# Performance work log

Hardware: AMD Instinct MI355X
Metric: run time of the kernel (lower is better)

The kernel has to match this reference:

```python
import jax, jax.numpy as jnp
import numpy as np

CUBE_LEN = 512
EQU_H = 1024
EQU_W = 2 * EQU_H
EQU_COUNT = 4
CHANNELS = 3


def _rodrigues(r):
    th = np.linalg.norm(r)
    if th < 1e-12:
        return np.eye(3)
    k = r / th
    K = np.array([[0.0, -k[2], k[1]], [k[2], 0.0, -k[0]], [-k[1], k[0], 0.0]])
    return np.eye(3) + np.sin(th) * K + (1.0 - np.cos(th)) * (K @ K)


def _build_lut(L, equ_h):
    # Identical math to Cube2Equirec.__init__/_intersection, fused into
    # per-pixel face id + per-pixel cube-face pixel coordinates (u, v).
    equ_w = equ_h * 2
    theta = (np.arange(equ_w) / (equ_w - 1) - 0.5) * 2 * np.pi
    phi = (np.arange(equ_h) / (equ_h - 1) - 0.5) * np.pi
    theta, phi = np.meshgrid(theta, phi)
    x = np.sin(theta) * np.cos(phi)
    y = np.sin(phi)
    z = np.cos(theta) * np.cos(phi)
    xyz = np.stack([x, y, z], axis=-1)  # [H, W, 3]
    planes = np.array([[0, 0, 1, -1], [1, 0, 0, -1], [0, 0, 1, 1],
                       [1, 0, 0, 1], [0, 1, 0, 1], [0, 1, 0, -1]], dtype=np.float64)
    r_lst = np.array([[0, 0, 0], [0, -0.5, 0], [0, 1, 0],
                      [0, 0.5, 0], [-0.5, 0, 0], [0.5, 0, 0]]) * np.pi
    f = L / 2.0
    K = np.array([[f, 0, (L - 1) / 2.0], [0, f, (L - 1) / 2.0], [0, 0, 1]])
    R_lst = np.stack([_rodrigues(r) for r in r_lst])  # [6, 3, 3]

    abc = planes[:, :3]
    with np.errstate(divide='ignore'):
        depth = -planes[:, 3][None, None, :] / (xyz @ abc.T)  # [H, W, 6]
    depth[depth < 0] = np.inf
    arg = np.argmin(depth, axis=-1)            # per-pixel face id
    dmin = np.min(depth, axis=-1)
    pts = dmin[..., None] * xyz                # intersection points
    Rs = R_lst[arg]                            # [H, W, 3, 3]
    proj = np.einsum('ij,hwjk,hwk->hwi', K, Rs, pts)  # K @ R @ pts
    uv = np.clip(proj[..., :2] / proj[..., 2:3], 0, L - 1)
    return uv.astype(np.float32), arg.astype(np.int32)


def setup_inputs() -> dict:
    key = jax.random.key(0)
    x = jax.random.normal(key, (6 * EQU_COUNT, CHANNELS, CUBE_LEN, CUBE_LEN),
                          dtype=jnp.float32)
    uv_np, face_np = _build_lut(CUBE_LEN, EQU_H)
    return {"x": x, "uv": jnp.asarray(uv_np), "face_idx": jnp.asarray(face_np)}


def _cube2equirec(x, uv, face_idx):
    # x: [6*E, C, L, L]; grid_sample(mode='bilinear', align_corners=True)
    # with grid = (uv/(L-1) - 0.5)*2 samples exactly at pixel coords uv.
    E6, C, L, _ = x.shape
    E = E6 // 6
    xr = x.reshape(E, 6, C, L, L)
    H, W = face_idx.shape
    f = face_idx.reshape(-1)                 # [N]
    u = uv[..., 0].reshape(-1)               # [N], in [0, L-1]
    v = uv[..., 1].reshape(-1)

    x0 = jnp.clip(jnp.floor(u).astype(jnp.int32), 0, L - 1)
    y0 = jnp.clip(jnp.floor(v).astype(jnp.int32), 0, L - 1)
    x1 = jnp.minimum(x0 + 1, L - 1)
    y1 = jnp.minimum(y0 + 1, L - 1)
    wx = (u - x0.astype(u.dtype))[:, None, None]  # [N,1,1]
    wy = (v - y0.astype(v.dtype))[:, None, None]

    def g(yy, xx):
        # advanced indices at axes 1,3,4 -> result [N, E, C]
        return xr[:, f, :, yy, xx]

    out = (g(y0, x0) * (1 - wx) * (1 - wy)
           + g(y0, x1) * wx * (1 - wy)
           + g(y1, x0) * (1 - wx) * wy
           + g(y1, x1) * wx * wy)              # [N, E, C]
    return jnp.transpose(out, (1, 2, 0)).reshape(E, C, H, W)


def reference(x, uv, face_idx):
    return _cube2equirec(x, uv, face_idx)
```

## Files before the change

### kernel.cpp

```cpp
#include <hip/hip_runtime.h>
#include <stdint.h>

#define EQU_H 1024
#define EQU_W 2048
#define HW (EQU_H * EQU_W)

typedef float f32x4 __attribute__((ext_vector_type(4)));
typedef float f32x2 __attribute__((ext_vector_type(2)));

#define IMG_OFF(i)  ((uint64_t)(((i) / 3) * 18874368u + ((i) % 3) * 1048576u))
#define IMG_FOFF(i) (((i) / 3) * 4718592 + ((i) % 3) * 262144)

__device__ __forceinline__ int wave_min(int v) {
#pragma unroll
    for (int o = 32; o; o >>= 1) v = min(v, __shfl_xor(v, o));
    return v;
}
__device__ __forceinline__ int wave_max(int v) {
#pragma unroll
    for (int o = 32; o; o >>= 1) v = max(v, __shfl_xor(v, o));
    return v;
}

__global__ __launch_bounds__(256, 1) void cube2equirec_kernel(
    const float* __restrict__ x,
    const float* __restrict__ uv,
    const int*   __restrict__ face,
    float*       __restrict__ out)
{
    __shared__ float slds[3][1600];
    __shared__ int   sred[24];

    const int ty = blockIdx.x & 63;
    const int tx = blockIdx.x >> 6;
    const int pr = threadIdx.x & 15;
    const int rw = threadIdx.x >> 4;
    const int w  = tx * 32 + pr * 2;
    const int h  = ty * 16 + rw;
    const int pidx = (h * EQU_W + w) >> 1;

    const f32x4 uv4 = ((const f32x4*)uv)[pidx];
    const int2  fpr = ((const int2*)face)[pidx];
    const float uA = uv4.x, vA = uv4.y, uB = uv4.z, vB = uv4.w;
    const int   fA = fpr.x, fB = fpr.y;

    int x0A = (int)floorf(uA), y0A = (int)floorf(vA);
    int x0B = (int)floorf(uB), y0B = (int)floorf(vB);
    x0A = min(max(x0A, 0), 510); y0A = min(max(y0A, 0), 510);
    x0B = min(max(x0B, 0), 510); y0B = min(max(y0B, 0), 510);
    const float wxA = uA - (float)x0A, wyA = vA - (float)y0A;
    const float wxB = uB - (float)x0B, wyB = vB - (float)y0B;

    int fmn = min(fA, fB),   fmx = max(fA, fB);
    int xmn = min(x0A, x0B), xmx = max(x0A, x0B);
    int ymn = min(y0A, y0B), ymx = max(y0A, y0B);
    fmn = wave_min(fmn); fmx = wave_max(fmx);
    xmn = wave_min(xmn); xmx = wave_max(xmx);
    ymn = wave_min(ymn); ymx = wave_max(ymx);
    const int wid = threadIdx.x >> 6, lane = threadIdx.x & 63;
    if (lane == 0) {
        int* p = &sred[wid * 6];
        p[0] = fmn; p[1] = fmx; p[2] = xmn; p[3] = xmx; p[4] = ymn; p[5] = ymx;
    }
    __syncthreads();
#pragma unroll
    for (int ww = 0; ww < 4; ++ww) {
        const int* p = &sred[ww * 6];
        fmn = min(fmn, p[0]); fmx = max(fmx, p[1]);
        xmn = min(xmn, p[2]); xmx = max(xmx, p[3]);
        ymn = min(ymn, p[4]); ymx = max(ymx, p[5]);
    }

    const int xs = xmn & ~3;
    const int R  = ymx + 2 - ymn;
    int C = ((xmx + 2 - xs) + 3) & ~3;
    C = min(C, 512 - xs);
    const int  U      = C >> 2;
    const bool staged = (fmn == fmx) && (U * R <= 400);
    const uint64_t xb = (uint64_t)x;

    if (staged) {
        const int UR = U * R;
        const int fbase = fmn * 786432;
        const int u0 = threadIdx.x, u1 = threadIdx.x + 256;
        const int r0 = u0 / U, c0 = u0 - r0 * U;
        const int r1 = u1 / U, c1 = u1 - r1 * U;
        const bool g0 = u0 < UR, g1 = u1 < UR;
        const int go0 = (ymn + r0) * 512 + xs + (c0 << 2);
        const int go1 = (ymn + r1) * 512 + xs + (c1 << 2);
        const int lo0 = r0 * C + (c0 << 2);
        const int lo1 = r1 * C + (c1 << 2);
        const int lA = (y0A - ymn) * C + (x0A - xs);
        const int lB = (y0B - ymn) * C + (x0B - xs);

        const float w00A = (1.f - wxA) * (1.f - wyA), w01A = wxA * (1.f - wyA);
        const float w10A = (1.f - wxA) * wyA,         w11A = wxA * wyA;
        const float w00B = (1.f - wxB) * (1.f - wyB), w01B = wxB * (1.f - wyB);
        const float w10B = (1.f - wxB) * wyB,         w11B = wxB * wyB;

#pragma unroll
        for (int k = 0; k < 4; ++k) {
#pragma unroll
            for (int r = 0; r < 3; ++r) {
                const float* src = x + IMG_FOFF(k * 3 + r) + fbase;
                if (g0) *((f32x4*)&slds[r][lo0]) = *(const f32x4*)(src + go0);
                if (g1) *((f32x4*)&slds[r][lo1]) = *(const f32x4*)(src + go1);
            }
            __syncthreads();
#pragma unroll
            for (int r = 0; r < 3; ++r) {
                const int i = k * 3 + r;
                const float* L = slds[r];
                const float a00 = L[lA], a01 = L[lA + 1];
                const float a10 = L[lA + C], a11 = L[lA + C + 1];
                const float b00 = L[lB], b01 = L[lB + 1];
                const float b10 = L[lB + C], b11 = L[lB + C + 1];
                f32x2 st;
                st.x = a00 * w00A + a01 * w01A + a10 * w10A + a11 * w11A;
                st.y = b00 * w00B + b01 * w01B + b10 * w10B + b11 * w11B;
                __builtin_nontemporal_store(st, (f32x2*)(out + (size_t)i * HW) + pidx);
            }
            __syncthreads();
        }
        return;
    }

    const int  xmw    = min(x0A, x0B);
    const bool compat = (fA == fB) && (y0A == y0B)
                     && ((max(x0A, x0B) - xmw) <= 2);
    const int xm  = min(compat ? xmw : x0A, 508);
    const int oAw = x0A - xm;
    const int oBw = min(max(x0B - xm, 0), 2);

    const uint32_t vbW = (uint32_t)(fA * 3145728 + y0A * 2048 + xm * 4);
    const uint32_t vbB = (uint32_t)(fB * 3145728 + y0B * 2048 + x0B * 4);

    const float aL = 1.f - wxA, aR = wxA;
    const float bL = 1.f - wxB, bR = wxB;
    f32x4 WA, WB;
    WA.x = (oAw == 0) ? aL : 0.f;
    WA.y = (oAw == 0) ? aR : ((oAw == 1) ? aL : 0.f);
    WA.z = (oAw == 2) ? aL : ((oAw == 1) ? aR : 0.f);
    WA.w = (oAw == 2) ? aR : 0.f;
    WB.x = (oBw == 0) ? bL : 0.f;
    WB.y = (oBw == 0) ? bR : ((oBw == 1) ? bL : 0.f);
    WB.z = (oBw == 2) ? bL : ((oBw == 1) ? bR : 0.f);
    WB.w = (oBw == 2) ? bR : 0.f;
    const f32x4 WA0 = WA * (1.f - wyA), WA1 = WA * wyA;
    const f32x4 WB0 = WB * (1.f - wyB), WB1 = WB * wyB;
    const float c00 = bL * (1.f - wyB), c01 = bR * (1.f - wyB);
    const float c10 = bL * wyB,         c11 = bR * wyB;

#define EMIT2(i, R0, R1, Q0, Q1)                                             \
    {                                                                        \
        const float ovA = R0.x * WA0.x + R0.y * WA0.y + R0.z * WA0.z         \
                        + R0.w * WA0.w + R1.x * WA1.x + R1.y * WA1.y         \
                        + R1.z * WA1.z + R1.w * WA1.w;                       \
        const float oBw2 = R0.x * WB0.x + R0.y * WB0.y + R0.z * WB0.z        \
                        + R0.w * WB0.w + R1.x * WB1.x + R1.y * WB1.y         \
                        + R1.z * WB1.z + R1.w * WB1.w;                       \
        const float oBf = Q0.x * c00 + Q0.y * c01 + Q1.x * c10 + Q1.y * c11; \
        f32x2 st;                                                            \
        st.x = ovA;                                                          \
        st.y = compat ? oBw2 : oBf;                                          \
        __builtin_nontemporal_store(st, (f32x2*)(out + (size_t)(i) * HW) + pidx); \
    }

#define ROUND(I0)                                                            \
    {                                                                        \
        f32x4 r0_0, r1_0, r0_1, r1_1, r0_2, r1_2,                            \
              r0_3, r1_3, r0_4, r1_4, r0_5, r1_5;                            \
        asm volatile(                                                        \
            "global_load_dwordx4 %[a0], %[vb], %[s0]\n\t"                    \
            "global_load_dwordx4 %[b0], %[vb], %[s0] offset:2048\n\t"        \
            "global_load_dwordx4 %[a1], %[vb], %[s1]\n\t"                    \
            "global_load_dwordx4 %[b1], %[vb], %[s1] offset:2048\n\t"        \
            "global_load_dwordx4 %[a2], %[vb], %[s2]\n\t"                    \
            "global_load_dwordx4 %[b2], %[vb], %[s2] offset:2048\n\t"        \
            "global_load_dwordx4 %[a3], %[vb], %[s3]\n\t"                    \
            "global_load_dwordx4 %[b3], %[vb], %[s3] offset:2048\n\t"        \
            "global_load_dwordx4 %[a4], %[vb], %[s4]\n\t"                    \
            "global_load_dwordx4 %[b4], %[vb], %[s4] offset:2048\n\t"        \
            "global_load_dwordx4 %[a5], %[vb], %[s5]\n\t"                    \
            "global_load_dwordx4 %[b5], %[vb], %[s5] offset:2048"            \
            : [a0] "=&v"(r0_0), [b0] "=&v"(r1_0),                            \
              [a1] "=&v"(r0_1), [b1] "=&v"(r1_1),                            \
              [a2] "=&v"(r0_2), [b2] "=&v"(r1_2),                            \
              [a3] "=&v"(r0_3), [b3] "=&v"(r1_3),                            \
              [a4] "=&v"(r0_4), [b4] "=&v"(r1_4),                            \
              [a5] "=&v"(r0_5), [b5] "=&v"(r1_5)                             \
            : [vb] "v"(vbW),                                                 \
              [s0] "s"(xb + IMG_OFF((I0) + 0)),                              \
              [s1] "s"(xb + IMG_OFF((I0) + 1)),                              \
              [s2] "s"(xb + IMG_OFF((I0) + 2)),                              \
              [s3] "s"(xb + IMG_OFF((I0) + 3)),                              \
              [s4] "s"(xb + IMG_OFF((I0) + 4)),                              \
              [s5] "s"(xb + IMG_OFF((I0) + 5)));                             \
        f32x2 q0_0 = {0.f, 0.f}, q1_0 = {0.f, 0.f};                          \
        f32x2 q0_1 = {0.f, 0.f}, q1_1 = {0.f, 0.f};                          \
        f32x2 q0_2 = {0.f, 0.f}, q1_2 = {0.f, 0.f};                          \
        f32x2 q0_3 = {0.f, 0.f}, q1_3 = {0.f, 0.f};                          \
        f32x2 q0_4 = {0.f, 0.f}, q1_4 = {0.f, 0.f};                          \
        f32x2 q0_5 = {0.f, 0.f}, q1_5 = {0.f, 0.f};                          \
        if (!compat) {                                                       \
            asm volatile(                                                    \
                "global_load_dwordx2 %[a0], %[vb], %[s0]\n\t"                \
                "global_load_dwordx2 %[b0], %[vb], %[s0] offset:2048\n\t"    \
                "global_load_dwordx2 %[a1], %[vb], %[s1]\n\t"                \
                "global_load_dwordx2 %[b1], %[vb], %[s1] offset:2048\n\t"    \
                "global_load_dwordx2 %[a2], %[vb], %[s2]\n\t"                \
                "global_load_dwordx2 %[b2], %[vb], %[s2] offset:2048\n\t"    \
                "global_load_dwordx2 %[a3], %[vb], %[s3]\n\t"                \
                "global_load_dwordx2 %[b3], %[vb], %[s3] offset:2048\n\t"    \
                "global_load_dwordx2 %[a4], %[vb], %[s4]\n\t"                \
                "global_load_dwordx2 %[b4], %[vb], %[s4] offset:2048\n\t"    \
                "global_load_dwordx2 %[a5], %[vb], %[s5]\n\t"                \
                "global_load_dwordx2 %[b5], %[vb], %[s5] offset:2048"        \
                : [a0] "=&v"(q0_0), [b0] "=&v"(q1_0),                        \
                  [a1] "=&v"(q0_1), [b1] "=&v"(q1_1),                        \
                  [a2] "=&v"(q0_2), [b2] "=&v"(q1_2),                        \
                  [a3] "=&v"(q0_3), [b3] "=&v"(q1_3),                        \
                  [a4] "=&v"(q0_4), [b4] "=&v"(q1_4),                        \
                  [a5] "=&v"(q0_5), [b5] "=&v"(q1_5)                         \
                : [vb] "v"(vbB),                                             \
                  [s0] "s"(xb + IMG_OFF((I0) + 0)),                          \
                  [s1] "s"(xb + IMG_OFF((I0) + 1)),                          \
                  [s2] "s"(xb + IMG_OFF((I0) + 2)),                          \
                  [s3] "s"(xb + IMG_OFF((I0) + 3)),                          \
                  [s4] "s"(xb + IMG_OFF((I0) + 4)),                          \
                  [s5] "s"(xb + IMG_OFF((I0) + 5)));                         \
        }                                                                    \
        asm volatile("s_waitcnt vmcnt(0)" ::: "memory");                     \
        __builtin_amdgcn_sched_barrier(0);                                   \
        EMIT2((I0) + 0, r0_0, r1_0, q0_0, q1_0)                              \
        EMIT2((I0) + 1, r0_1, r1_1, q0_1, q1_1)                              \
        EMIT2((I0) + 2, r0_2, r1_2, q0_2, q1_2)                              \
        EMIT2((I0) + 3, r0_3, r1_3, q0_3, q1_3)                              \
        EMIT2((I0) + 4, r0_4, r1_4, q0_4, q1_4)                              \
        EMIT2((I0) + 5, r0_5, r1_5, q0_5, q1_5)                              \
    }

    ROUND(0)
    ROUND(6)

#undef ROUND
#undef EMIT2
}

extern "C" void kernel_launch(void* const* d_in, const int* in_sizes, int n_in,
                              void* d_out, int out_size, void* d_ws, size_t ws_size,
                              hipStream_t stream) {
    const float* x    = (const float*)d_in[0];
    const float* uv   = (const float*)d_in[1];
    const int*   face = (const int*)d_in[2];
    float*       out  = (float*)d_out;

    const int grid = 64 * 64;
    hipLaunchKernelGGL(cube2equirec_kernel, dim3(grid), dim3(256), 0, stream,
                       x, uv, face, out);
}
```

Baseline: 214.3 us.

## Register-prefetch next batch's cube tiles while computing current batch in staged path

```diff
diff --git a/kernel.cpp b/kernel.cpp
--- a/kernel.cpp
+++ b/kernel.cpp
@@ -28,7 +28,7 @@
     const int*   __restrict__ face,
     float*       __restrict__ out)
 {
-    __shared__ float slds[3][1600];
+    __shared__ float slds[3][2048];
     __shared__ int   sred[24];
 
     const int ty = blockIdx.x & 63;
@@ -76,7 +76,7 @@
     int C = ((xmx + 2 - xs) + 3) & ~3;
     C = min(C, 512 - xs);
     const int  U      = C >> 2;
-    const bool staged = (fmn == fmx) && (U * R <= 400);
+    const bool staged = (fmn == fmx) && (U * R <= 512);
     const uint64_t xb = (uint64_t)x;
 
     if (staged) {
@@ -98,15 +98,46 @@
         const float w00B = (1.f - wxB) * (1.f - wyB), w01B = wxB * (1.f - wyB);
         const float w10B = (1.f - wxB) * wyB,         w11B = wxB * wyB;
 
+        f32x4 p0_0, p0_1, p0_2, p1_0, p1_1, p1_2;
+#define PREF(K)                                                              \
+        {                                                                    \
+            const float* s0_ = x + IMG_FOFF((K) * 3 + 0) + fbase;            \
+            const float* s1_ = x + IMG_FOFF((K) * 3 + 1) + fbase;            \
+            const float* s2_ = x + IMG_FOFF((K) * 3 + 2) + fbase;            \
+            if (g0) {                                                        \
+                p0_0 = *(const f32x4*)(s0_ + go0);                           \
+                p0_1 = *(const f32x4*)(s1_ + go0);                           \
+                p0_2 = *(const f32x4*)(s2_ + go0);                           \
+            }                                                                \
+            if (g1) {                                                        \
+                p1_0 = *(const f32x4*)(s0_ + go1);                           \
+                p1_1 = *(const f32x4*)(s1_ + go1);                           \
+                p1_2 = *(const f32x4*)(s2_ + go1);                           \
+            }                                                                \
+        }
+        PREF(0)
+
 #pragma unroll
         for (int k = 0; k < 4; ++k) {
-#pragma unroll
-            for (int r = 0; r < 3; ++r) {
-                const float* src = x + IMG_FOFF(k * 3 + r) + fbase;
-                if (g0) *((f32x4*)&slds[r][lo0]) = *(const f32x4*)(src + go0);
-                if (g1) *((f32x4*)&slds[r][lo1]) = *(const f32x4*)(src + go1);
+            if (g0) {
+                *((f32x4*)&slds[0][lo0]) = p0_0;
+                *((f32x4*)&slds[1][lo0]) = p0_1;
+                *((f32x4*)&slds[2][lo0]) = p0_2;
+            }
+            if (g1) {
+                *((f32x4*)&slds[0][lo1]) = p1_0;
+                *((f32x4*)&slds[1][lo1]) = p1_1;
+                *((f32x4*)&slds[2][lo1]) = p1_2;
             }
             __syncthreads();
+            if (k < 3) {
+                switch (k) {
+                case 0: PREF(1) break;
+                case 1: PREF(2) break;
+                default: PREF(3) break;
+                }
+                __builtin_amdgcn_sched_barrier(0);
+            }
 #pragma unroll
             for (int r = 0; r < 3; ++r) {
                 const int i = k * 3 + r;
@@ -123,6 +154,7 @@
             __syncthreads();
         }
         return;
+#undef PREF
     }
 
     const int  xmw    = min(x0A, x0B);
```

Result: faster. 195.1 us (-9.0%).
